# Performance work log

Measured on AMD Instinct MI355X. Metric: run time of the kernel, lower is better.

## Reference

```python
import jax, jax.numpy as jnp
import numpy as np

EPS = 1e-5
GROUPS = 32


def group_norm(x, gamma, beta):
    # x: [B, C, H, W], normalize per group over (C/G, H, W)
    B, C, H, W = x.shape
    xg = x.reshape(B, GROUPS, C // GROUPS, H, W)
    mean = xg.mean(axis=(2, 3, 4), keepdims=True)
    var = xg.var(axis=(2, 3, 4), keepdims=True)
    xg = (xg - mean) * jax.lax.rsqrt(var + EPS)
    x = xg.reshape(B, C, H, W)
    return x * gamma[None, :, None, None] + beta[None, :, None, None]


def setup_inputs() -> dict:
    key = jax.random.key(0)
    ks = jax.random.split(key, 6)
    B, C, H, W = 8, 512, 64, 64
    x = jax.random.normal(ks[0], (B, C, H, W), dtype=jnp.float32)
    gamma = jnp.ones((C,), dtype=jnp.float32)
    beta = jnp.zeros((C,), dtype=jnp.float32)
    # conv1x1 weights stored as [out, in] (kernel size 1 squeezed)
    w_qkv = jax.random.normal(ks[1], (3 * C, C), dtype=jnp.float32) / np.sqrt(C)
    b_qkv = jnp.zeros((3 * C,), dtype=jnp.float32)
    w_out = jax.random.normal(ks[2], (C, C), dtype=jnp.float32) / np.sqrt(C)
    b_out = jnp.zeros((C,), dtype=jnp.float32)
    return {"x": x, "gamma": gamma, "beta": beta,
            "w_qkv": w_qkv, "b_qkv": b_qkv, "w_out": w_out, "b_out": b_out}


def reference(x, gamma, beta, w_qkv, b_qkv, w_out, b_out):
    B, C, H, W = x.shape
    N = H * W
    h = group_norm(x, gamma, beta).reshape(B, C, N)
    # conv1d kernel-size-1: channel mixing
    qkv = jnp.einsum('oc,bcn->bon', w_qkv, h) + b_qkv[None, :, None]
    q, k, v = jnp.split(qkv, 3, axis=1)  # each [B, C, N]
    scale = 1.0 / jnp.sqrt(jnp.float32(C))
    attn = jnp.einsum('bci,bcj->bij', q, k) * scale  # [B, N, N]
    attn = jax.nn.softmax(attn, axis=-1)
    out = jnp.einsum('bcj,bij->bci', v, attn)  # [B, C, N]
    out = jnp.einsum('oc,bcn->bon', w_out, out) + b_out[None, :, None]
    return x + out.reshape(B, C, H, W)
```

## Files before the change

kernel.cpp:

```cpp
#include <hip/hip_runtime.h>

#define BB 8
#define CC 512
#define NN 4096
#define GG 32
#define OQKV 1536
#define EPSV 1e-5f
#define SCALE 0.044194173824159216f

#define BATCH_STRIDE 6291456u
#define V_OFF 0u
#define Q_OFF 2097152u
#define K_OFF 4194304u

typedef unsigned short u16;
typedef unsigned int u32;
typedef __attribute__((ext_vector_type(8))) short bf16x8;
typedef __attribute__((ext_vector_type(4))) float f32x4;

#define FOR16(OP) OP(0) OP(1) OP(2) OP(3) OP(4) OP(5) OP(6) OP(7) \
                  OP(8) OP(9) OP(10) OP(11) OP(12) OP(13) OP(14) OP(15)

__device__ __forceinline__ u16 f2bf(float f) {
  u32 u = __float_as_uint(f);
  u32 r = (u + 0x7FFFu + ((u >> 16) & 1u)) >> 16;
  return (u16)r;
}

__device__ __forceinline__ u32 pack2bf(float a, float b) {
  return (u32)f2bf(a) | ((u32)f2bf(b) << 16);
}

__device__ __forceinline__ void gload_lds16(const u16* g, u16* l) {
  __builtin_amdgcn_global_load_lds(
      (const __attribute__((address_space(1))) u32*)(g),
      (__attribute__((address_space(3))) u32*)(l), 16, 0, 0);
}

__global__ __launch_bounds__(256) void gn_stats_kernel(const float* __restrict__ x,
                                                       float* __restrict__ stats) {
  const int bg = blockIdx.x;
  const float4* xp = (const float4*)(x + (size_t)bg * 16 * NN);
  const int n4 = 16 * NN / 4;
  float s = 0.f, ss = 0.f;
  for (int i = threadIdx.x; i < n4; i += 256) {
    float4 v = xp[i];
    s += v.x + v.y + v.z + v.w;
    ss += v.x * v.x + v.y * v.y + v.z * v.z + v.w * v.w;
  }
  for (int off = 32; off > 0; off >>= 1) {
    s += __shfl_down(s, off, 64);
    ss += __shfl_down(ss, off, 64);
  }
  __shared__ float rs[4], rss[4];
  const int wid = threadIdx.x >> 6, lane = threadIdx.x & 63;
  if (lane == 0) { rs[wid] = s; rss[wid] = ss; }
  __syncthreads();
  if (threadIdx.x == 0) {
    float S = rs[0] + rs[1] + rs[2] + rs[3];
    float SS = rss[0] + rss[1] + rss[2] + rss[3];
    const float invn = 1.0f / (16.0f * NN);
    float mean = S * invn;
    float var = SS * invn - mean * mean;
    stats[bg * 2] = mean;
    stats[bg * 2 + 1] = rsqrtf(var + EPSV);
  }
}

__global__ __launch_bounds__(256) void gn_transpose_kernel(
    const float* __restrict__ x, const float* __restrict__ gamma,
    const float* __restrict__ beta, const float* __restrict__ stats,
    u16* __restrict__ hT) {
  __shared__ __align__(16) u16 Ts[64 * 64];
  const int b = blockIdx.z;
  const int c0 = blockIdx.y * 64;
  const int n0 = blockIdx.x * 64;
  const int t = threadIdx.x;
  const float* xb = x + ((size_t)b * CC + c0) * NN;
#pragma unroll
  for (int it = 0; it < 2; ++it) {
    const int U = it * 256 + t;
    const int r = U >> 3, cu = U & 7;
    const int c = c0 + r;
    const int g = c >> 4;
    const float mean = stats[(b * GG + g) * 2];
    const float rstd = stats[(b * GG + g) * 2 + 1];
    const float aa = rstd * gamma[c];
    const float dd = beta[c] - mean * aa;
    const float* src = xb + (size_t)r * NN + n0 + cu * 8;
    float4 v0 = *(const float4*)src;
    float4 v1 = *(const float4*)(src + 4);
    uint4 pk;
    pk.x = pack2bf(fmaf(aa, v0.x, dd), fmaf(aa, v0.y, dd));
    pk.y = pack2bf(fmaf(aa, v0.z, dd), fmaf(aa, v0.w, dd));
    pk.z = pack2bf(fmaf(aa, v1.x, dd), fmaf(aa, v1.y, dd));
    pk.w = pack2bf(fmaf(aa, v1.z, dd), fmaf(aa, v1.w, dd));
    const int pu = cu ^ ((r >> 3) & 7);
    *(uint4*)((char*)Ts + r * 128 + pu * 16) = pk;
  }
  __syncthreads();
#pragma unroll
  for (int it = 0; it < 2; ++it) {
    const int U = it * 256 + t;
    const int n = U >> 3, cu2 = U & 7;
    bf16x8 v;
#pragma unroll
    for (int jj = 0; jj < 8; ++jj) {
      const int c = cu2 * 8 + jj;
      v[jj] = (short)Ts[c * 64 + (((n >> 3) ^ cu2) << 3) + (n & 7)];
    }
    *(bf16x8*)(hT + ((size_t)b * NN + n0 + n) * CC + c0 + cu2 * 8) = v;
  }
}

__global__ __launch_bounds__(256) void convert_w_kernel(const float* __restrict__ w,
                                                        u16* __restrict__ wb, int n8) {
  const int i = blockIdx.x * 256 + threadIdx.x;
  if (i >= n8) return;
  const float4 a = *(const float4*)(w + (size_t)i * 8);
  const float4 b = *(const float4*)(w + (size_t)i * 8 + 4);
  uint4 pk;
  pk.x = pack2bf(a.x, a.y);
  pk.y = pack2bf(a.z, a.w);
  pk.z = pack2bf(b.x, b.y);
  pk.w = pack2bf(b.z, b.w);
  *(uint4*)(wb + (size_t)i * 8) = pk;
}

__global__ __launch_bounds__(256) void qkv_mfma_kernel(
    const u16* __restrict__ hT, const u16* __restrict__ wbf,
    const float* __restrict__ bqkv, u16* __restrict__ qkv) {
  __shared__ __align__(16) u16 Asb[128 * 32 * 2];
  u16* const Bsb = Asb + 128 * 32;
  const int b = blockIdx.z;
  const int o0 = blockIdx.y * 128;
  const int n0 = blockIdx.x * 128;
  const int t = threadIdx.x;
  const int w = t >> 6;
  const int lane = t & 63;
  const int quad = lane >> 4;
  const int m16 = lane & 15;
  const int wm = w >> 1, wn = w & 1;

  const int sr = lane >> 2;
  const int gu = (lane & 3) ^ ((lane >> 3) & 3);
  const u16* gA0 = wbf + (size_t)(o0 + w * 32 + sr) * CC + gu * 8;
  const u16* gA1 = gA0 + (size_t)16 * CC;
  const u16* hTb = hT + (size_t)b * NN * CC;
  const u16* gB0 = hTb + (size_t)(n0 + w * 32 + sr) * CC + gu * 8;
  const u16* gB1 = gB0 + (size_t)16 * CC;
  u16* const lA0 = Asb + (w * 32) * 32;
  u16* const lA1 = Asb + (w * 32 + 16) * 32;
  u16* const lB0 = Bsb + (w * 32) * 32;
  u16* const lB1 = Bsb + (w * 32 + 16) * 32;

  const int sfr = (m16 >> 1) & 3;
  const u16* aP[4];
  const u16* bP[4];
#pragma unroll
  for (int mt = 0; mt < 4; ++mt)
    aP[mt] = Asb + (wm * 64 + mt * 16 + m16) * 32 + (quad ^ sfr) * 8;
#pragma unroll
  for (int ct = 0; ct < 4; ++ct)
    bP[ct] = Bsb + (wn * 64 + ct * 16 + m16) * 32 + (quad ^ sfr) * 8;

  f32x4 acc[4][4];
#pragma unroll
  for (int mt = 0; mt < 4; ++mt)
#pragma unroll
    for (int ct = 0; ct < 4; ++ct) acc[mt][ct] = (f32x4){0.f, 0.f, 0.f, 0.f};

  for (int kk = 0; kk < 16; ++kk) {
    __syncthreads();
    gload_lds16(gA0, lA0);
    gload_lds16(gA1, lA1);
    gload_lds16(gB0, lB0);
    gload_lds16(gB1, lB1);
    gA0 += 32; gA1 += 32; gB0 += 32; gB1 += 32;
    __syncthreads();
    bf16x8 af[4], bfr[4];
#pragma unroll
    for (int mt = 0; mt < 4; ++mt) af[mt] = *(const bf16x8*)aP[mt];
#pragma unroll
    for (int ct = 0; ct < 4; ++ct) bfr[ct] = *(const bf16x8*)bP[ct];
#pragma unroll
    for (int mt = 0; mt < 4; ++mt)
#pragma unroll
      for (int ct = 0; ct < 4; ++ct)
        acc[mt][ct] = __builtin_amdgcn_mfma_f32_16x16x32_bf16(af[mt], bfr[ct],
                                                              acc[mt][ct], 0, 0, 0);
  }
  __syncthreads();

  u16* qb = qkv + (size_t)b * BATCH_STRIDE;
  size_t roff;
  int lo0;
  if (o0 < 512) { roff = Q_OFF; lo0 = o0; }
  else if (o0 < 1024) { roff = K_OFF; lo0 = o0 - 512; }
  else { roff = V_OFF; lo0 = o0 - 1024; }

  u16* const scr = Asb + w * 1024;
#pragma unroll
  for (int mt = 0; mt < 4; ++mt) {
#pragma unroll
    for (int ct = 0; ct < 4; ++ct) {
#pragma unroll
      for (int i = 0; i < 4; ++i) {
        const int row = quad * 4 + i;
        const int nn = ct * 16 + m16;
        const int pu = (nn >> 3) ^ ((row & 7) ^ (row >> 3));
        scr[row * 64 + pu * 8 + (nn & 7)] =
            f2bf(acc[mt][ct][i] + bqkv[o0 + wm * 64 + mt * 16 + row]);
      }
    }
    __syncthreads();
#pragma unroll
    for (int half = 0; half < 2; ++half) {
      const int idx = half * 64 + lane;
      const int row = idx >> 3;
      const int cu = idx & 7;
      const int pu = cu ^ ((row & 7) ^ (row >> 3));
      bf16x8 vv = *(const bf16x8*)(scr + row * 64 + pu * 8);
      *(bf16x8*)(qb + roff + (size_t)(lo0 + wm * 64 + mt * 16 + row) * NN +
                 n0 + wn * 64 + cu * 8) = vv;
    }
    __syncthreads();
  }
}

__global__ __launch_bounds__(256) void transpose_qk_kernel(
    const u16* __restrict__ qkvbuf, u16* __restrict__ qT, u16* __restrict__ kT) {
  __shared__ __align__(16) u16 Ts[64 * 64];
  const int b = blockIdx.z >> 1;
  const int which = blockIdx.z & 1;
  const int c0 = blockIdx.y * 64;
  const int n0 = blockIdx.x * 64;
  const int t = threadIdx.x;
  const u16* src = qkvbuf + (size_t)b * BATCH_STRIDE + (which ? K_OFF : Q_OFF);
  u16* dst = (which ? kT : qT) + (size_t)b * (CC * NN);
#pragma unroll
  for (int it = 0; it < 2; ++it) {
    const int U = it * 256 + t;
    const int r = U >> 3, cu = U & 7;
    const int pu = cu ^ ((r >> 3) & 7);
    *(uint4*)((char*)Ts + r * 128 + pu * 16) =
        *(const uint4*)(src + (size_t)(c0 + r) * NN + n0 + cu * 8);
  }
  __syncthreads();
#pragma unroll
  for (int it = 0; it < 2; ++it) {
    const int U = it * 256 + t;
    const int n = U >> 3, cu2 = U & 7;
    bf16x8 v;
#pragma unroll
    for (int jj = 0; jj < 8; ++jj) {
      const int c = cu2 * 8 + jj;
      v[jj] = (short)Ts[c * 64 + (((n >> 3) ^ cu2) << 3) + (n & 7)];
    }
    *(bf16x8*)(dst + (size_t)(n0 + n) * CC + c0 + cu2 * 8) = v;
  }
}

__global__ __launch_bounds__(512, 1) void attn_mfma_kernel(
    u16* __restrict__ qkvbuf, const u16* __restrict__ qT, const u16* __restrict__ kT) {
  __shared__ __align__(16) u16 smem[70656];
  u16* const Qs = smem;
  u16* const Kt = smem + 32768;
  u16* const Vt = smem + 49152;
  u16* const Pbase = smem + 65536;

  const int flat = blockIdx.y * 64 + blockIdx.x;
  const int b = flat & 7;
  const int i0 = (flat >> 3) * 64;
  const int t = threadIdx.x;
  const int w = t >> 6;
  const int lane = t & 63;
  const int quad = lane >> 4;
  const int m16 = lane & 15;
  const int wq = w >> 1;
  const int wc = w & 1;

  const u16* vb = qkvbuf + (size_t)b * BATCH_STRIDE + V_OFF;
  float* obuf = (float*)(qkvbuf + (size_t)b * BATCH_STRIDE + Q_OFF);
  const u16* qTb = qT + (size_t)b * (CC * NN);
  const u16* kTb = kT + (size_t)b * (CC * NN);
  u16* const myP = Pbase + w * 640;

  const int vsrcu = ((lane & 3) ^ ((lane >> 2) & 3)) * 8;
  const int vrow = lane >> 2;

#pragma unroll
  for (int it = 0; it < 8; ++it) {
    const int r = it * 8 + w;
    gload_lds16(qTb + (size_t)(i0 + r) * CC + (lane ^ (r & 7)) * 8,
                Qs + r * 512 + lane * 8);
  }
  uint4 kst[4], vst[4];
#pragma unroll
  for (int it = 0; it < 4; ++it) {
    const int j = it * 8 + w;
    kst[it] = *(const uint4*)(kTb + (size_t)j * CC + (lane ^ (j & 7)) * 8);
  }
#pragma unroll
  for (int it = 0; it < 4; ++it) {
    const int c = (it * 8 + w) * 16 + vrow;
    vst[it] = *(const uint4*)(vb + (size_t)c * NN + vsrcu);
  }
#pragma unroll
  for (int it = 0; it < 4; ++it)
    *(uint4*)(Kt + (it * 8 + w) * 512 + lane * 8) = kst[it];
#pragma unroll
  for (int it = 0; it < 4; ++it)
    *(uint4*)(Vt + (it * 8 + w) * 512 + lane * 8) = vst[it];

  float m_r = -1e30f, l_r = 0.f;
#define ODECL(ct) f32x4 o##ct = (f32x4){0.f, 0.f, 0.f, 0.f};
  FOR16(ODECL)
#undef ODECL

  __syncthreads();

  const u16* const Qrow = Qs + (wq * 16 + m16) * 512;
  const u16* const k0 = Kt + m16 * 512;
  const u16* const k1 = k0 + 16 * 512;
  const u16* const vbase = Vt + wc * 8192 + m16 * 32 + (quad ^ (m16 & 3)) * 8;
  const int sz = m16 & 7;

  for (int jt = 0; jt < NN / 32; ++jt) {
    f32x4 s0 = (f32x4){0.f, 0.f, 0.f, 0.f};
    f32x4 s1 = (f32x4){0.f, 0.f, 0.f, 0.f};
#define SSTEP(kc) { const int u = ((kc * 4 + quad) ^ sz) * 8; \
      bf16x8 qf = *(const bf16x8*)(Qrow + u); \
      bf16x8 ka = *(const bf16x8*)(k0 + u); \
      bf16x8 kb = *(const bf16x8*)(k1 + u); \
      s0 = __builtin_amdgcn_mfma_f32_16x16x32_bf16(ka, qf, s0, 0, 0, 0); \
      s1 = __builtin_amdgcn_mfma_f32_16x16x32_bf16(kb, qf, s1, 0, 0, 0); }
    FOR16(SSTEP)
#undef SSTEP
    if (jt + 1 < NN / 32) {
      const int j0n = (jt + 1) * 32;
#pragma unroll
      for (int it = 0; it < 4; ++it) {
        const int j = it * 8 + w;
        kst[it] = *(const uint4*)(kTb + (size_t)(j0n + j) * CC + (lane ^ (j & 7)) * 8);
      }
#pragma unroll
      for (int it = 0; it < 4; ++it) {
        const int c = (it * 8 + w) * 16 + vrow;
        vst[it] = *(const uint4*)(vb + (size_t)c * NN + j0n + vsrcu);
      }
    }
    float p0 = s0[0] * SCALE, p1 = s0[1] * SCALE, p2 = s0[2] * SCALE, p3 = s0[3] * SCALE;
    float p4 = s1[0] * SCALE, p5 = s1[1] * SCALE, p6 = s1[2] * SCALE, p7 = s1[3] * SCALE;
    float mx = fmaxf(fmaxf(fmaxf(p0, p1), fmaxf(p2, p3)),
                     fmaxf(fmaxf(p4, p5), fmaxf(p6, p7)));
    mx = fmaxf(mx, __shfl_xor(mx, 16));
    mx = fmaxf(mx, __shfl_xor(mx, 32));
    const float mold = m_r;
    const float mnew = fmaxf(mold, mx);
    m_r = mnew;
    const float alpha = __expf(mold - mnew);
    p0 = __expf(p0 - mnew); p1 = __expf(p1 - mnew);
    p2 = __expf(p2 - mnew); p3 = __expf(p3 - mnew);
    p4 = __expf(p4 - mnew); p5 = __expf(p5 - mnew);
    p6 = __expf(p6 - mnew); p7 = __expf(p7 - mnew);
    float sum = ((p0 + p1) + (p2 + p3)) + ((p4 + p5) + (p6 + p7));
    sum += __shfl_xor(sum, 16);
    sum += __shfl_xor(sum, 32);
    l_r = l_r * alpha + sum;
    uint2 pw0, pw1;
    pw0.x = pack2bf(p0, p1); pw0.y = pack2bf(p2, p3);
    pw1.x = pack2bf(p4, p5); pw1.y = pack2bf(p6, p7);
    *(uint2*)(myP + m16 * 40 + quad * 4) = pw0;
    *(uint2*)(myP + m16 * 40 + 16 + quad * 4) = pw1;
    asm volatile("s_waitcnt lgkmcnt(0)" ::: "memory");
    bf16x8 pf = *(const bf16x8*)(myP + m16 * 40 + quad * 8);
    const float a0 = __shfl(alpha, quad * 4 + 0);
    const float a1 = __shfl(alpha, quad * 4 + 1);
    const float a2 = __shfl(alpha, quad * 4 + 2);
    const float a3 = __shfl(alpha, quad * 4 + 3);
    const bool nores = __all(mnew == mold);
#define PVN(ct) { bf16x8 vf = *(const bf16x8*)(vbase + ct * 512); \
      o##ct = __builtin_amdgcn_mfma_f32_16x16x32_bf16(pf, vf, o##ct, 0, 0, 0); }
#define PVR(ct) { bf16x8 vf = *(const bf16x8*)(vbase + ct * 512); \
      f32x4 oo = o##ct; oo[0] *= a0; oo[1] *= a1; oo[2] *= a2; oo[3] *= a3; \
      o##ct = __builtin_amdgcn_mfma_f32_16x16x32_bf16(pf, vf, oo, 0, 0, 0); }
    if (nores) {
      FOR16(PVN)
    } else {
      FOR16(PVR)
    }
#undef PVN
#undef PVR
    __syncthreads();
    if (jt + 1 < NN / 32) {
#pragma unroll
      for (int it = 0; it < 4; ++it)
        *(uint4*)(Kt + (it * 8 + w) * 512 + lane * 8) = kst[it];
#pragma unroll
      for (int it = 0; it < 4; ++it)
        *(uint4*)(Vt + (it * 8 + w) * 512 + lane * 8) = vst[it];
    }
    __syncthreads();
  }
  const float invl = 1.0f / l_r;
  const float il0 = __shfl(invl, quad * 4 + 0);
  const float il1 = __shfl(invl, quad * 4 + 1);
  const float il2 = __shfl(invl, quad * 4 + 2);
  const float il3 = __shfl(invl, quad * 4 + 3);
  const size_t ncol = i0 + wq * 16 + quad * 4;
#define EPI(ct) { float4 ov; \
      ov.x = o##ct[0] * il0; ov.y = o##ct[1] * il1; \
      ov.z = o##ct[2] * il2; ov.w = o##ct[3] * il3; \
      *(float4*)(obuf + (size_t)(wc * 256 + ct * 16 + m16) * NN + ncol) = ov; }
  FOR16(EPI)
#undef EPI
}

__global__ __launch_bounds__(256) void proj_kernel(
    const u16* __restrict__ qkvbuf, const float* __restrict__ wout,
    const float* __restrict__ bout, const float* __restrict__ x,
    float* __restrict__ out) {
  __shared__ __align__(16) float Wt[16][68];
  __shared__ __align__(16) float Ht[16][68];
  const int b = blockIdx.z;
  const int o0 = blockIdx.y * 64;
  const int n0 = blockIdx.x * 64;
  const int t = threadIdx.x;
  const int to = (t >> 4) * 4;
  const int tn = (t & 15) * 4;
  const int wo = t >> 2;
  const int wk = (t & 3) * 4;
  const int xc = t >> 4;
  const int xn = (t & 15) * 4;
  const float* ob = (const float*)(qkvbuf + (size_t)b * BATCH_STRIDE + Q_OFF);
  float acc[4][4] = {{0.f}};
  for (int kk = 0; kk < CC; kk += 16) {
    float4 wv = *(const float4*)(wout + (size_t)(o0 + wo) * CC + kk + wk);
    float4 hv = *(const float4*)(ob + (size_t)(kk + xc) * NN + n0 + xn);
    __syncthreads();
    Wt[wk + 0][wo] = wv.x;
    Wt[wk + 1][wo] = wv.y;
    Wt[wk + 2][wo] = wv.z;
    Wt[wk + 3][wo] = wv.w;
    *(float4*)&Ht[xc][xn] = hv;
    __syncthreads();
#pragma unroll
    for (int k = 0; k < 16; ++k) {
      float4 w4 = *(const float4*)&Wt[k][to];
      float4 h4 = *(const float4*)&Ht[k][tn];
      acc[0][0] = fmaf(w4.x, h4.x, acc[0][0]);
      acc[0][1] = fmaf(w4.x, h4.y, acc[0][1]);
      acc[0][2] = fmaf(w4.x, h4.z, acc[0][2]);
      acc[0][3] = fmaf(w4.x, h4.w, acc[0][3]);
      acc[1][0] = fmaf(w4.y, h4.x, acc[1][0]);
      acc[1][1] = fmaf(w4.y, h4.y, acc[1][1]);
      acc[1][2] = fmaf(w4.y, h4.z, acc[1][2]);
      acc[1][3] = fmaf(w4.y, h4.w, acc[1][3]);
      acc[2][0] = fmaf(w4.z, h4.x, acc[2][0]);
      acc[2][1] = fmaf(w4.z, h4.y, acc[2][1]);
      acc[2][2] = fmaf(w4.z, h4.z, acc[2][2]);
      acc[2][3] = fmaf(w4.z, h4.w, acc[2][3]);
      acc[3][0] = fmaf(w4.w, h4.x, acc[3][0]);
      acc[3][1] = fmaf(w4.w, h4.y, acc[3][1]);
      acc[3][2] = fmaf(w4.w, h4.z, acc[3][2]);
      acc[3][3] = fmaf(w4.w, h4.w, acc[3][3]);
    }
  }
#pragma unroll
  for (int i = 0; i < 4; ++i) {
    const int o = o0 + to + i;
    const float bias = bout[o];
    const size_t idx = ((size_t)b * CC + o) * NN + n0 + tn;
    float4 xv = *(const float4*)(x + idx);
    float4 r;
    r.x = acc[i][0] + bias + xv.x;
    r.y = acc[i][1] + bias + xv.y;
    r.z = acc[i][2] + bias + xv.z;
    r.w = acc[i][3] + bias + xv.w;
    *(float4*)(out + idx) = r;
  }
}

extern "C" void kernel_launch(void* const* d_in, const int* in_sizes, int n_in,
                              void* d_out, int out_size, void* d_ws, size_t ws_size,
                              hipStream_t stream) {
  const float* x = (const float*)d_in[0];
  const float* gamma = (const float*)d_in[1];
  const float* beta = (const float*)d_in[2];
  const float* wqkv = (const float*)d_in[3];
  const float* bqkv = (const float*)d_in[4];
  const float* wout = (const float*)d_in[5];
  const float* bout = (const float*)d_in[6];
  float* out = (float*)d_out;

  char* ws = (char*)d_ws;
  float* stats = (float*)ws;
  u16* qkv = (u16*)(ws + 4096);
  u16* qT = (u16*)(ws + 4096 + (size_t)BB * OQKV * NN * 2);
  u16* kT = qT + (size_t)BB * CC * NN;
  u16* hT = qT;
  u16* wbf = kT;

  gn_stats_kernel<<<BB * GG, 256, 0, stream>>>(x, stats);
  gn_transpose_kernel<<<dim3(NN / 64, CC / 64, BB), 256, 0, stream>>>(
      x, gamma, beta, stats, hT);
  convert_w_kernel<<<(OQKV * CC / 8 + 255) / 256, 256, 0, stream>>>(
      wqkv, wbf, OQKV * CC / 8);
  qkv_mfma_kernel<<<dim3(NN / 128, OQKV / 128, BB), 256, 0, stream>>>(
      hT, wbf, bqkv, qkv);
  transpose_qk_kernel<<<dim3(NN / 64, CC / 64, BB * 2), 256, 0, stream>>>(qkv, qT, kT);
  attn_mfma_kernel<<<dim3(NN / 64, BB), 512, 0, stream>>>(qkv, qT, kT);
  proj_kernel<<<dim3(NN / 64, CC / 64, BB), 256, 0, stream>>>(qkv, wout, bout, x, out);
}
```

Before: 1.843 ms.

## Double-buffer K via direct LDS loads, read V from global, split QK across warp pairs

K tiles now go straight to LDS through async global-to-LDS loads into two alternating buffers, replacing the register-staged K/V copies. V fragments are read directly from global memory in the PV MFMA loop instead of being staged in LDS. The QK^T work is split between paired warps, each computing one 16-column half and exchanging scores through a new LDS scratch area, with a barrier added mid-iteration. This cuts duplicated QK MFMAs and LDS staging at the cost of uncoalesced global V reads and an extra sync per tile.

```diff
diff --git a/kernel.cpp b/kernel.cpp
--- a/kernel.cpp
+++ b/kernel.cpp
@@ -263,11 +263,12 @@
 
 __global__ __launch_bounds__(512, 1) void attn_mfma_kernel(
     u16* __restrict__ qkvbuf, const u16* __restrict__ qT, const u16* __restrict__ kT) {
-  __shared__ __align__(16) u16 smem[70656];
+  __shared__ __align__(16) u16 smem[74752];
   u16* const Qs = smem;
-  u16* const Kt = smem + 32768;
-  u16* const Vt = smem + 49152;
+  u16* const KtA = smem + 32768;
+  u16* const KtB = smem + 49152;
   u16* const Pbase = smem + 65536;
+  float* const Sx = (float*)(smem + 70656);
 
   const int flat = blockIdx.y * 64 + blockIdx.x;
   const int b = flat & 7;
@@ -285,9 +286,8 @@
   const u16* qTb = qT + (size_t)b * (CC * NN);
   const u16* kTb = kT + (size_t)b * (CC * NN);
   u16* const myP = Pbase + w * 640;
-
-  const int vsrcu = ((lane & 3) ^ ((lane >> 2) & 3)) * 8;
-  const int vrow = lane >> 2;
+  float* const mySx = Sx + w * 256;
+  const float* const otSx = Sx + (w ^ 1) * 256;
 
 #pragma unroll
   for (int it = 0; it < 8; ++it) {
@@ -295,23 +295,11 @@
     gload_lds16(qTb + (size_t)(i0 + r) * CC + (lane ^ (r & 7)) * 8,
                 Qs + r * 512 + lane * 8);
   }
-  uint4 kst[4], vst[4];
 #pragma unroll
   for (int it = 0; it < 4; ++it) {
     const int j = it * 8 + w;
-    kst[it] = *(const uint4*)(kTb + (size_t)j * CC + (lane ^ (j & 7)) * 8);
-  }
-#pragma unroll
-  for (int it = 0; it < 4; ++it) {
-    const int c = (it * 8 + w) * 16 + vrow;
-    vst[it] = *(const uint4*)(vb + (size_t)c * NN + vsrcu);
-  }
-#pragma unroll
-  for (int it = 0; it < 4; ++it)
-    *(uint4*)(Kt + (it * 8 + w) * 512 + lane * 8) = kst[it];
-#pragma unroll
-  for (int it = 0; it < 4; ++it)
-    *(uint4*)(Vt + (it * 8 + w) * 512 + lane * 8) = vst[it];
+    gload_lds16(kTb + (size_t)j * CC + (lane ^ (j & 7)) * 8, KtA + j * 512 + lane * 8);
+  }
 
   float m_r = -1e30f, l_r = 0.f;
 #define ODECL(ct) f32x4 o##ct = (f32x4){0.f, 0.f, 0.f, 0.f};
@@ -321,35 +309,37 @@
   __syncthreads();
 
   const u16* const Qrow = Qs + (wq * 16 + m16) * 512;
-  const u16* const k0 = Kt + m16 * 512;
-  const u16* const k1 = k0 + 16 * 512;
-  const u16* const vbase = Vt + wc * 8192 + m16 * 32 + (quad ^ (m16 & 3)) * 8;
   const int sz = m16 & 7;
+  const int krow = wc * 16 + m16;
+  const u16* const vrow_g = vb + (size_t)(wc * 256 + m16) * NN + quad * 8;
 
   for (int jt = 0; jt < NN / 32; ++jt) {
-    f32x4 s0 = (f32x4){0.f, 0.f, 0.f, 0.f};
-    f32x4 s1 = (f32x4){0.f, 0.f, 0.f, 0.f};
+    const u16* Ktc = (jt & 1) ? KtB : KtA;
+    u16* Ktn = (jt & 1) ? KtA : KtB;
+    if (jt + 1 < NN / 32) {
+      const int j0n = (jt + 1) * 32;
+#pragma unroll
+      for (int it = 0; it < 4; ++it) {
+        const int j = it * 8 + w;
+        gload_lds16(kTb + (size_t)(j0n + j) * CC + (lane ^ (j & 7)) * 8,
+                    Ktn + j * 512 + lane * 8);
+      }
+    }
+    f32x4 sh = (f32x4){0.f, 0.f, 0.f, 0.f};
+    {
+      const u16* kh = Ktc + krow * 512;
 #define SSTEP(kc) { const int u = ((kc * 4 + quad) ^ sz) * 8; \
       bf16x8 qf = *(const bf16x8*)(Qrow + u); \
-      bf16x8 ka = *(const bf16x8*)(k0 + u); \
-      bf16x8 kb = *(const bf16x8*)(k1 + u); \
-      s0 = __builtin_amdgcn_mfma_f32_16x16x32_bf16(ka, qf, s0, 0, 0, 0); \
-      s1 = __builtin_amdgcn_mfma_f32_16x16x32_bf16(kb, qf, s1, 0, 0, 0); }
-    FOR16(SSTEP)
+      bf16x8 ka = *(const bf16x8*)(kh + u); \
+      sh = __builtin_amdgcn_mfma_f32_16x16x32_bf16(ka, qf, sh, 0, 0, 0); }
+      FOR16(SSTEP)
 #undef SSTEP
-    if (jt + 1 < NN / 32) {
-      const int j0n = (jt + 1) * 32;
-#pragma unroll
-      for (int it = 0; it < 4; ++it) {
-        const int j = it * 8 + w;
-        kst[it] = *(const uint4*)(kTb + (size_t)(j0n + j) * CC + (lane ^ (j & 7)) * 8);
-      }
-#pragma unroll
-      for (int it = 0; it < 4; ++it) {
-        const int c = (it * 8 + w) * 16 + vrow;
-        vst[it] = *(const uint4*)(vb + (size_t)c * NN + j0n + vsrcu);
-      }
-    }
+    }
+    *(f32x4*)(mySx + m16 * 16 + quad * 4) = sh;
+    __syncthreads();
+    f32x4 so = *(const f32x4*)(otSx + m16 * 16 + quad * 4);
+    f32x4 s0 = wc ? so : sh;
+    f32x4 s1 = wc ? sh : so;
     float p0 = s0[0] * SCALE, p1 = s0[1] * SCALE, p2 = s0[2] * SCALE, p3 = s0[3] * SCALE;
     float p4 = s1[0] * SCALE, p5 = s1[1] * SCALE, p6 = s1[2] * SCALE, p7 = s1[3] * SCALE;
     float mx = fmaxf(fmaxf(fmaxf(p0, p1), fmaxf(p2, p3)),
@@ -379,10 +369,11 @@
     const float a1 = __shfl(alpha, quad * 4 + 1);
     const float a2 = __shfl(alpha, quad * 4 + 2);
     const float a3 = __shfl(alpha, quad * 4 + 3);
+    const u16* vg = vrow_g + jt * 32;
     const bool nores = __all(mnew == mold);
-#define PVN(ct) { bf16x8 vf = *(const bf16x8*)(vbase + ct * 512); \
+#define PVN(ct) { bf16x8 vf = *(const bf16x8*)(vg + (size_t)(ct * 16) * NN); \
       o##ct = __builtin_amdgcn_mfma_f32_16x16x32_bf16(pf, vf, o##ct, 0, 0, 0); }
-#define PVR(ct) { bf16x8 vf = *(const bf16x8*)(vbase + ct * 512); \
+#define PVR(ct) { bf16x8 vf = *(const bf16x8*)(vg + (size_t)(ct * 16) * NN); \
       f32x4 oo = o##ct; oo[0] *= a0; oo[1] *= a1; oo[2] *= a2; oo[3] *= a3; \
       o##ct = __builtin_amdgcn_mfma_f32_16x16x32_bf16(pf, vf, oo, 0, 0, 0); }
     if (nores) {
@@ -392,15 +383,6 @@
     }
 #undef PVN
 #undef PVR
-    __syncthreads();
-    if (jt + 1 < NN / 32) {
-#pragma unroll
-      for (int it = 0; it < 4; ++it)
-        *(uint4*)(Kt + (it * 8 + w) * 512 + lane * 8) = kst[it];
-#pragma unroll
-      for (int it = 0; it < 4; ++it)
-        *(uint4*)(Vt + (it * 8 + w) * 512 + lane * 8) = vst[it];
-    }
     __syncthreads();
   }
   const float invl = 1.0f / l_r;
```

Result: faster. 1.803 ms (-2.2%).
